# Performance work log

Hardware: AMD Instinct MI355X
Metric: run time of the kernel (lower is better)

The kernel has to match this reference:

```python
import jax, jax.numpy as jnp
import numpy as np
import math

B, S, D, H = 2, 2048, 1024, 16
DK = D // H


def setup_inputs() -> dict:
    key = jax.random.key(0)
    ks = jax.random.split(key, 12)
    std = 1.0 / math.sqrt(D)
    inp = {
        "q": jax.random.normal(ks[0], (B, S, D), jnp.float32),
        "k": jax.random.normal(ks[1], (B, S, D), jnp.float32),
        "v": jax.random.normal(ks[2], (B, S, D), jnp.float32),
        # causal mask, broadcast over batch and heads
        "mask": jnp.tril(jnp.ones((S, S), jnp.int32))[None, None, :, :],
        "wq": jax.random.normal(ks[3], (D, D), jnp.float32) * std,
        "bq": jax.random.normal(ks[4], (D,), jnp.float32) * std,
        "wk": jax.random.normal(ks[5], (D, D), jnp.float32) * std,
        "bk": jax.random.normal(ks[6], (D,), jnp.float32) * std,
        "wv": jax.random.normal(ks[7], (D, D), jnp.float32) * std,
        "bv": jax.random.normal(ks[8], (D,), jnp.float32) * std,
        "wo": jax.random.normal(ks[9], (D, D), jnp.float32) * std,
        "bo": jax.random.normal(ks[10], (D,), jnp.float32) * std,
    }
    return inp


def _split_heads(x):
    # [B,S,D] -> [B,H,S,DK]
    b, s, _ = x.shape
    return x.reshape(b, s, H, DK).transpose(0, 2, 1, 3)


def reference(q, k, v, mask, wq, bq, wk, bk, wv, bv, wo, bo):
    # nn.Linear: y = x @ W^T + b
    query = _split_heads(q @ wq.T + bq)
    key_h = _split_heads(k @ wk.T + bk)
    value = _split_heads(v @ wv.T + bv)

    scale = 1.0 / math.sqrt(DK)
    scores = jnp.einsum("bhqd,bhkd->bhqk", query, key_h) * scale  # [B,H,S,S]
    scores = jnp.where(mask == 0, jnp.float32(-1e9), scores)
    attn = jax.nn.softmax(scores, axis=-1)  # dropout p=0.0 -> identity

    x = jnp.einsum("bhqk,bhkd->bhqd", attn, value)  # [B,H,S,DK]
    x = x.transpose(0, 2, 1, 3).reshape(q.shape[0], -1, H * DK)  # [B,S,D]
    return x @ wo.T + bo
```

## Files before the change

### kernel.cpp

```cpp
#include <hip/hip_runtime.h>

#define B_SZ    2
#define S_LEN   2048
#define D_MODEL 1024
#define H_NUM   16
#define DK_H    64
#define M_ROWS  (B_SZ * S_LEN)

typedef __attribute__((ext_vector_type(8))) short  short8;
typedef __attribute__((ext_vector_type(4))) short  short4v;
typedef __attribute__((ext_vector_type(4))) float  floatx4;

__device__ __forceinline__ short f2b(float f) {
    union { float f; unsigned u; } x; x.f = f;
    unsigned u = x.u + 0x7fffu + ((x.u >> 16) & 1u);
    return (short)(u >> 16);
}

typedef __attribute__((address_space(1))) const unsigned int gu32;
typedef __attribute__((address_space(3))) unsigned int       lu32;
__device__ __forceinline__ void gload_lds16(const short* g, short* l) {
    __builtin_amdgcn_global_load_lds((gu32*)g, (lu32*)l, 16, 0, 0);
}

#define QSCALE 0.18033688011112042f
#define SM_SHIFT 12.0f

__global__ void cvt_all_kernel(const float* __restrict__ xq, const float* __restrict__ xk,
                               const float* __restrict__ xv, const float* __restrict__ wq,
                               const float* __restrict__ wk, const float* __restrict__ wv,
                               const float* __restrict__ wo,
                               short* __restrict__ oxq, short* __restrict__ oxk,
                               short* __restrict__ oxv, short* __restrict__ owq,
                               short* __restrict__ owk, short* __restrict__ owv,
                               short* __restrict__ owo)
{
    const int y = blockIdx.y;
    const float* in;
    short* out;
    switch (y) {
        case 0: in = xq; out = oxq; break;
        case 1: in = xk; out = oxk; break;
        case 2: in = xv; out = oxv; break;
        case 3: in = wq; out = owq; break;
        case 4: in = wk; out = owk; break;
        case 5: in = wv; out = owv; break;
        default: in = wo; out = owo; break;
    }
    int base = blockIdx.x * 1024 + threadIdx.x * 4;
    if (y < 3) {
        for (int p = 0; p < 4; ++p) {
            int i = base + p * 1048576;
            float4 v = *(const float4*)(in + i);
            short4v r;
            r[0] = f2b(v.x); r[1] = f2b(v.y); r[2] = f2b(v.z); r[3] = f2b(v.w);
            *(short4v*)(out + i) = r;
        }
    } else {
        int i = base;
        int n = i >> 10, k = i & 1023;
        float4 v = *(const float4*)(in + i);
        short4v r;
        r[0] = f2b(v.x); r[1] = f2b(v.y); r[2] = f2b(v.z); r[3] = f2b(v.w);
        *(short4v*)(out + (((n >> 4) * 128 + (k >> 3)) * 128 + (n & 15) * 8 + (k & 4))) = r;
    }
}

__global__ __launch_bounds__(256, 2)
void gemm_qkv_kernel(const short* __restrict__ xq, const short* __restrict__ xk,
                     const short* __restrict__ xv,
                     const short* __restrict__ wq, const short* __restrict__ wk,
                     const short* __restrict__ wv,
                     const float* __restrict__ bq, const float* __restrict__ bk,
                     const float* __restrict__ bv,
                     short* __restrict__ Qp, short* __restrict__ Kp, short* __restrict__ Vt)
{
    __shared__ short sa[128 * 32];

    const int which = blockIdx.y >> 3;
    const short* A    = (which == 0) ? xq : (which == 1) ? xk : xv;
    const short* W    = (which == 0) ? wq : (which == 1) ? wk : wv;
    const float* bias = (which == 0) ? bq : (which == 1) ? bk : bv;
    const float scale = (which == 0) ? QSCALE : 1.0f;

    const int nb = (blockIdx.y & 7) * 128;
    const int m0 = blockIdx.x * 128;
    const int t = threadIdx.x, wave = t >> 6, lane = t & 63;
    const int quad = lane >> 4, l16 = lane & 15;
    const int wm = (wave & 1) * 64, wn = (wave >> 1) * 64;

    const int r0 = t >> 2, cs = t & 3;
    const int c0 = cs ^ ((r0 >> 1) & 3);
    const short* Ab0 = A + (size_t)(m0 + r0) * D_MODEL + c0 * 8;
    const short* Ab1 = Ab0 + (size_t)64 * D_MODEL;
    short* sa0 = sa + t * 8;  short* sa1 = sa + 2048 + t * 8;

    int a_off[4];
#pragma unroll
    for (int i = 0; i < 4; ++i) {
        int ar = wm + i * 16 + l16;
        a_off[i] = ar * 32 + ((quad ^ ((ar >> 1) & 3)) * 8);
    }

    const short* Wt = W + ((size_t)((nb + wn) >> 4) * 128 + quad) * 128 + l16 * 8;

#define LOADB(dst, k0) do { _Pragma("unroll")                                  \
    for (int nt_ = 0; nt_ < 4; ++nt_)                                          \
        dst[nt_] = *(const short8*)(Wt + nt_ * 16384 + (k0) * 16); } while (0)

    short8 bfA[4], bfB[4];
    LOADB(bfA, 0);

    floatx4 acc[4][4] = {};
#pragma unroll 1
    for (int k0 = 0; k0 < D_MODEL; k0 += 64) {
        __syncthreads();
        gload_lds16(Ab0 + k0, sa0);
        gload_lds16(Ab1 + k0, sa1);
        __syncthreads();
        LOADB(bfB, k0 + 32);
#pragma unroll
        for (int mt = 0; mt < 4; ++mt) {
            short8 af = *(const short8*)(sa + a_off[mt]);
#pragma unroll
            for (int nt = 0; nt < 4; ++nt)
                acc[mt][nt] = __builtin_amdgcn_mfma_f32_16x16x32_bf16(af, bfA[nt], acc[mt][nt], 0, 0, 0);
        }
        __syncthreads();
        gload_lds16(Ab0 + k0 + 32, sa0);
        gload_lds16(Ab1 + k0 + 32, sa1);
        __syncthreads();
        if (k0 + 64 < D_MODEL) LOADB(bfA, k0 + 64);
#pragma unroll
        for (int mt = 0; mt < 4; ++mt) {
            short8 af = *(const short8*)(sa + a_off[mt]);
#pragma unroll
            for (int nt = 0; nt < 4; ++nt)
                acc[mt][nt] = __builtin_amdgcn_mfma_f32_16x16x32_bf16(af, bfB[nt], acc[mt][nt], 0, 0, 0);
        }
    }
#undef LOADB

#pragma unroll
    for (int nt = 0; nt < 4; ++nt) {
        int ncol = nb + wn + nt * 16 + l16;
        int h = ncol >> 6, dk = ncol & 63;
        float bv_ = bias[ncol];
#pragma unroll
        for (int mt = 0; mt < 4; ++mt) {
            int mrow0 = m0 + wm + mt * 16 + quad * 4;
            int bb = mrow0 >> 11, s0 = mrow0 & (S_LEN - 1);
            if (which < 2) {
                short* Out = (which == 0) ? Qp : Kp;
#pragma unroll
                for (int r = 0; r < 4; ++r) {
                    float v = (acc[mt][nt][r] + bv_) * scale;
                    Out[(((size_t)bb * H_NUM + h) * S_LEN + (s0 + r)) * DK_H + dk] = f2b(v);
                }
            } else {
                int Sb = s0 & ~63, sb0_ = s0 & 63;
                size_t rowbase = (((size_t)bb * H_NUM + h) * DK_H + dk) * S_LEN + Sb;
#pragma unroll
                for (int r = 0; r < 4; ++r) {
                    int cc = sb0_ + r;
                    Vt[rowbase + ((cc & 15) * 4 + (cc >> 4))] = f2b(acc[mt][nt][r] + bv_);
                }
            }
        }
    }
}

__global__ __launch_bounds__(512, 4)
void attn_kernel(const short* __restrict__ Qp, const short* __restrict__ Kp,
                 const short* __restrict__ Vt, short* __restrict__ Xa)
{
    __shared__ short kbuf[2][64 * 64];
    __shared__ short vbuf[2][64 * 64];
    __shared__ short pl[8][16 * 72];

    const int lin = (int)(blockIdx.x + 16 * blockIdx.y);
    const int bh = lin & 31;
    const int j8 = (lin >> 5) & 7;
    const int tile = (lin >> 8) ? (15 - j8) : j8;

    const int t = threadIdx.x, wave = t >> 6, lane = t & 63;
    const int quad = lane >> 4, l16 = lane & 15;

    const short* Qb  = Qp + (size_t)bh * S_LEN * DK_H;
    const short* Kb  = Kp + (size_t)bh * S_LEN * DK_H;
    const short* Vtb = Vt + (size_t)bh * DK_H * S_LEN;

    const int q0 = tile * 128 + wave * 16;
    const int my_ktimax = 2 * tile + (wave >> 2);
    const int ktb = 2 * tile + 1;

    const int r0 = t >> 3, cs = t & 7;
    const int c0 = cs ^ (r0 & 7);
    const short* Kg = Kb + r0 * DK_H + c0 * 8;
    const short* Vg = Vtb + (size_t)r0 * S_LEN + c0 * 8;
    short* kl0 = &kbuf[0][t * 8]; short* kl1 = &kbuf[1][t * 8];
    short* vl0 = &vbuf[0][t * 8]; short* vl1 = &vbuf[1][t * 8];

    short8 qf[2];
#pragma unroll
    for (int ks = 0; ks < 2; ++ks)
        qf[ks] = *(const short8*)(Qb + (size_t)(q0 + l16) * DK_H + ks * 32 + quad * 8);

    short8 bl = {};
    if (l16 == 0) {
#pragma unroll
        for (int j = 0; j < 8; ++j) bl[j] = (short)0x3F80;
    }

    int fo[4][2];
#pragma unroll
    for (int nt = 0; nt < 4; ++nt)
#pragma unroll
        for (int ks = 0; ks < 2; ++ks) {
            int row = nt * 16 + l16;
            fo[nt][ks] = row * 64 + (((ks * 4 + quad) ^ (l16 & 7)) * 8);
        }

    floatx4 o[4] = {};
    floatx4 ol = {};
    short* plw = &pl[wave][0];
    const int qg = q0 + quad * 4;

    gload_lds16(Kg, kl0);
    gload_lds16(Vg, vl0);
    __syncthreads();

    for (int kti = 0; kti <= ktb; ++kti) {
        const short* kb = (kti & 1) ? &kbuf[1][0] : &kbuf[0][0];
        const short* vb = (kti & 1) ? &vbuf[1][0] : &vbuf[0][0];
        const int kbase = kti * 64;

        if (kti < ktb) {
            gload_lds16(Kg + (size_t)(kbase + 64) * DK_H, (kti & 1) ? kl0 : kl1);
            gload_lds16(Vg + (kbase + 64),                (kti & 1) ? vl0 : vl1);
        }

        if (kti <= my_ktimax) {
            short8 bkf[4][2];
#pragma unroll
            for (int nt = 0; nt < 4; ++nt)
#pragma unroll
                for (int ks = 0; ks < 2; ++ks)
                    bkf[nt][ks] = *(const short8*)(kb + fo[nt][ks]);

            floatx4 sc[4] = {};
#pragma unroll
            for (int nt = 0; nt < 4; ++nt)
#pragma unroll
                for (int ks = 0; ks < 2; ++ks)
                    sc[nt] = __builtin_amdgcn_mfma_f32_16x16x32_bf16(qf[ks], bkf[nt][ks], sc[nt], 0, 0, 0);

            if (kti == my_ktimax) {
#pragma unroll
                for (int nt = 0; nt < 4; ++nt) {
                    int key = kbase + nt * 16 + l16;
#pragma unroll
                    for (int r = 0; r < 4; ++r)
                        if (key > qg + r) sc[nt][r] = -1e30f;
                }
            }

#pragma unroll
            for (int r = 0; r < 4; ++r) {
                union { float f; unsigned u; } a0, a1, a2, a3;
                a0.f = exp2f(sc[0][r] - SM_SHIFT);
                a1.f = exp2f(sc[1][r] - SM_SHIFT);
                a2.f = exp2f(sc[2][r] - SM_SHIFT);
                a3.f = exp2f(sc[3][r] - SM_SHIFT);
                uint2 d;
                d.x = (a1.u & 0xffff0000u) | (a0.u >> 16);
                d.y = (a3.u & 0xffff0000u) | (a2.u >> 16);
                *(uint2*)(plw + (quad * 4 + r) * 72 + l16 * 4) = d;
            }

            short8 ap0 = *(const short8*)(plw + l16 * 72 + quad * 8);
            short8 ap1 = *(const short8*)(plw + l16 * 72 + 32 + quad * 8);

            short8 bvf[4][2];
#pragma unroll
            for (int nt = 0; nt < 4; ++nt)
#pragma unroll
                for (int ks = 0; ks < 2; ++ks)
                    bvf[nt][ks] = *(const short8*)(vb + fo[nt][ks]);

#pragma unroll
            for (int nt = 0; nt < 4; ++nt) {
                o[nt] = __builtin_amdgcn_mfma_f32_16x16x32_bf16(ap0, bvf[nt][0], o[nt], 0, 0, 0);
                o[nt] = __builtin_amdgcn_mfma_f32_16x16x32_bf16(ap1, bvf[nt][1], o[nt], 0, 0, 0);
            }
            ol = __builtin_amdgcn_mfma_f32_16x16x32_bf16(ap0, bl, ol, 0, 0, 0);
            ol = __builtin_amdgcn_mfma_f32_16x16x32_bf16(ap1, bl, ol, 0, 0, 0);
        }

        __syncthreads();
    }

    const int b_ = bh >> 4, h = bh & 15;
#pragma unroll
    for (int r = 0; r < 4; ++r) {
        float lsum = __shfl(ol[r], (lane & 48));
        float rinv = 1.0f / lsum;
        int srow = qg + r;
#pragma unroll
        for (int nt = 0; nt < 4; ++nt) {
            int col = h * 64 + nt * 16 + l16;
            Xa[((size_t)b_ * S_LEN + srow) * D_MODEL + col] = f2b(o[nt][r] * rinv);
        }
    }
}

__global__ __launch_bounds__(256, 2)
void gemm_out_kernel(const short* __restrict__ A, const short* __restrict__ W,
                     const float* __restrict__ bias, float* __restrict__ out)
{
    __shared__ short sa[128 * 32];

    const int nb = blockIdx.y * 64;
    const int m0 = blockIdx.x * 128;
    const int t = threadIdx.x, wave = t >> 6, lane = t & 63;
    const int quad = lane >> 4, l16 = lane & 15;
    const int wm = (wave & 1) * 64, wn = (wave >> 1) * 32;

    const int r0 = t >> 2, cs = t & 3;
    const int c0 = cs ^ ((r0 >> 1) & 3);
    const short* Ab0 = A + (size_t)(m0 + r0) * D_MODEL + c0 * 8;
    const short* Ab1 = Ab0 + (size_t)64 * D_MODEL;
    short* sa0 = sa + t * 8;  short* sa1 = sa + 2048 + t * 8;

    int a_off[4];
#pragma unroll
    for (int i = 0; i < 4; ++i) {
        int ar = wm + i * 16 + l16;
        a_off[i] = ar * 32 + ((quad ^ ((ar >> 1) & 3)) * 8);
    }

    const short* Wt = W + ((size_t)((nb + wn) >> 4) * 128 + quad) * 128 + l16 * 8;

#define LOADB2(dst, k0) do { _Pragma("unroll")                                 \
    for (int nt_ = 0; nt_ < 2; ++nt_)                                          \
        dst[nt_] = *(const short8*)(Wt + nt_ * 16384 + (k0) * 16); } while (0)

    short8 bfA[2], bfB[2];
    LOADB2(bfA, 0);

    floatx4 acc[4][2] = {};
#pragma unroll 1
    for (int k0 = 0; k0 < D_MODEL; k0 += 64) {
        __syncthreads();
        gload_lds16(Ab0 + k0, sa0);
        gload_lds16(Ab1 + k0, sa1);
        __syncthreads();
        LOADB2(bfB, k0 + 32);
#pragma unroll
        for (int mt = 0; mt < 4; ++mt) {
            short8 af = *(const short8*)(sa + a_off[mt]);
#pragma unroll
            for (int nt = 0; nt < 2; ++nt)
                acc[mt][nt] = __builtin_amdgcn_mfma_f32_16x16x32_bf16(af, bfA[nt], acc[mt][nt], 0, 0, 0);
        }
        __syncthreads();
        gload_lds16(Ab0 + k0 + 32, sa0);
        gload_lds16(Ab1 + k0 + 32, sa1);
        __syncthreads();
        if (k0 + 64 < D_MODEL) LOADB2(bfA, k0 + 64);
#pragma unroll
        for (int mt = 0; mt < 4; ++mt) {
            short8 af = *(const short8*)(sa + a_off[mt]);
#pragma unroll
            for (int nt = 0; nt < 2; ++nt)
                acc[mt][nt] = __builtin_amdgcn_mfma_f32_16x16x32_bf16(af, bfB[nt], acc[mt][nt], 0, 0, 0);
        }
    }
#undef LOADB2

#pragma unroll
    for (int nt = 0; nt < 2; ++nt) {
        int ncol = nb + wn + nt * 16 + l16;
        float bv_ = bias[ncol];
#pragma unroll
        for (int mt = 0; mt < 4; ++mt) {
            int mrow0 = m0 + wm + mt * 16 + quad * 4;
#pragma unroll
            for (int r = 0; r < 4; ++r)
                out[(size_t)(mrow0 + r) * D_MODEL + ncol] = acc[mt][nt][r] + bv_;
        }
    }
}

extern "C" void kernel_launch(void* const* d_in, const int* in_sizes, int n_in,
                              void* d_out, int out_size, void* d_ws, size_t ws_size,
                              hipStream_t stream)
{
    (void)in_sizes; (void)n_in; (void)out_size; (void)ws_size;
    const float* q  = (const float*)d_in[0];
    const float* k  = (const float*)d_in[1];
    const float* v  = (const float*)d_in[2];
    const float* wq = (const float*)d_in[4];
    const float* bq = (const float*)d_in[5];
    const float* wk = (const float*)d_in[6];
    const float* bk = (const float*)d_in[7];
    const float* wv = (const float*)d_in[8];
    const float* bv = (const float*)d_in[9];
    const float* wo = (const float*)d_in[10];
    const float* bo = (const float*)d_in[11];
    float* out = (float*)d_out;

    const size_t XE = (size_t)M_ROWS * D_MODEL;
    const size_t WE = (size_t)D_MODEL * D_MODEL;
    short* ws_  = (short*)d_ws;
    short* xq_b = ws_;
    short* xk_b = xq_b + XE;
    short* xv_b = xk_b + XE;
    short* wq_b = xv_b + XE;
    short* wk_b = wq_b + WE;
    short* wv_b = wk_b + WE;
    short* wo_b = wv_b + WE;
    short* Qp   = wo_b + WE;
    short* Kp   = Qp + XE;
    short* Vt   = Kp + XE;
    short* Xa   = xq_b;

    dim3 blk(256);
    cvt_all_kernel<<<dim3(1024, 7), blk, 0, stream>>>(
        q, k, v, wq, wk, wv, wo, xq_b, xk_b, xv_b, wq_b, wk_b, wv_b, wo_b);

    gemm_qkv_kernel<<<dim3(M_ROWS / 128, 24), blk, 0, stream>>>(
        xq_b, xk_b, xv_b, wq_b, wk_b, wv_b, bq, bk, bv, Qp, Kp, Vt);

    attn_kernel<<<dim3(16, B_SZ * H_NUM), dim3(512), 0, stream>>>(Qp, Kp, Vt, Xa);

    gemm_out_kernel<<<dim3(M_ROWS / 128, D_MODEL / 64), blk, 0, stream>>>(Xa, wo_b, bo, out);
}
```

Baseline: 232.1 us.

## Double-buffer A tiles in LDS for projection GEMMs and coalesce weight repack

The QKV and output GEMMs now stage the full 64-wide K slab of A into one of two LDS buffers with an XOR swizzle. The next slab is prefetched while the current one is consumed, which replaces four barriers per iteration with one. The weight conversion kernel is also rewritten so each thread reads 8 contiguous floats and writes a contiguous short8 in the packed layout. In exchange, LDS use per block grows fourfold, which could limit occupancy.

```diff
diff --git a/kernel.cpp b/kernel.cpp
--- a/kernel.cpp
+++ b/kernel.cpp
@@ -47,8 +47,8 @@
         case 5: in = wv; out = owv; break;
         default: in = wo; out = owo; break;
     }
-    int base = blockIdx.x * 1024 + threadIdx.x * 4;
     if (y < 3) {
+        int base = blockIdx.x * 1024 + threadIdx.x * 4;
         for (int p = 0; p < 4; ++p) {
             int i = base + p * 1048576;
             float4 v = *(const float4*)(in + i);
@@ -57,12 +57,18 @@
             *(short4v*)(out + i) = r;
         }
     } else {
-        int i = base;
-        int n = i >> 10, k = i & 1023;
-        float4 v = *(const float4*)(in + i);
-        short4v r;
-        r[0] = f2b(v.x); r[1] = f2b(v.y); r[2] = f2b(v.z); r[3] = f2b(v.w);
-        *(short4v*)(out + (((n >> 4) * 128 + (k >> 3)) * 128 + (n & 15) * 8 + (k & 4))) = r;
+        int f = blockIdx.x * 256 + (int)threadIdx.x;
+        if (blockIdx.x < 512) {
+            int n4 = f >> 11, rem = f & 2047;
+            int k8 = rem >> 4, nl = rem & 15;
+            const float* src = in + (size_t)(n4 * 16 + nl) * D_MODEL + k8 * 8;
+            float4 v0 = *(const float4*)(src);
+            float4 v1 = *(const float4*)(src + 4);
+            short8 r;
+            r[0] = f2b(v0.x); r[1] = f2b(v0.y); r[2] = f2b(v0.z); r[3] = f2b(v0.w);
+            r[4] = f2b(v1.x); r[5] = f2b(v1.y); r[6] = f2b(v1.z); r[7] = f2b(v1.w);
+            *(short8*)(out + (size_t)f * 8) = r;
+        }
     }
 }
 
@@ -75,7 +81,7 @@
                      const float* __restrict__ bv,
                      short* __restrict__ Qp, short* __restrict__ Kp, short* __restrict__ Vt)
 {
-    __shared__ short sa[128 * 32];
+    __shared__ short sa[2][128 * 64];
 
     const int which = blockIdx.y >> 3;
     const short* A    = (which == 0) ? xq : (which == 1) ? xk : xv;
@@ -89,17 +95,24 @@
     const int quad = lane >> 4, l16 = lane & 15;
     const int wm = (wave & 1) * 64, wn = (wave >> 1) * 64;
 
-    const int r0 = t >> 2, cs = t & 3;
-    const int c0 = cs ^ ((r0 >> 1) & 3);
-    const short* Ab0 = A + (size_t)(m0 + r0) * D_MODEL + c0 * 8;
-    const short* Ab1 = Ab0 + (size_t)64 * D_MODEL;
-    short* sa0 = sa + t * 8;  short* sa1 = sa + 2048 + t * 8;
-
-    int a_off[4];
+    const int rs = t >> 3;
+    const int cl = (t & 7) ^ (rs & 7);
+    const short* Asrc = A + (size_t)(m0 + rs) * D_MODEL + cl * 8;
+    short* sd0 = &sa[0][t * 8];
+    short* sd1 = &sa[1][t * 8];
+
+#define STAGE_A(dst, k0) do { _Pragma("unroll")                                \
+    for (int j_ = 0; j_ < 4; ++j_)                                             \
+        gload_lds16(Asrc + (size_t)j_ * 32 * D_MODEL + (k0),                   \
+                    (dst) + j_ * 2048); } while (0)
+
+    int a_off[4][2];
 #pragma unroll
     for (int i = 0; i < 4; ++i) {
         int ar = wm + i * 16 + l16;
-        a_off[i] = ar * 32 + ((quad ^ ((ar >> 1) & 3)) * 8);
+#pragma unroll
+        for (int ks = 0; ks < 2; ++ks)
+            a_off[i][ks] = ar * 64 + (((ks * 4 + quad) ^ (ar & 7)) * 8);
     }
 
     const short* Wt = W + ((size_t)((nb + wn) >> 4) * 128 + quad) * 128 + l16 * 8;
@@ -109,36 +122,38 @@
         dst[nt_] = *(const short8*)(Wt + nt_ * 16384 + (k0) * 16); } while (0)
 
     short8 bfA[4], bfB[4];
+    STAGE_A(sd0, 0);
     LOADB(bfA, 0);
+    __syncthreads();
 
     floatx4 acc[4][4] = {};
 #pragma unroll 1
     for (int k0 = 0; k0 < D_MODEL; k0 += 64) {
+        const int p = (k0 >> 6) & 1;
+        const short* cur = &sa[p][0];
+        if (k0 + 64 < D_MODEL) STAGE_A(p ? sd0 : sd1, k0 + 64);
+        LOADB(bfB, k0 + 32);
+
+        short8 af[4][2];
+#pragma unroll
+        for (int mt = 0; mt < 4; ++mt) {
+            af[mt][0] = *(const short8*)(cur + a_off[mt][0]);
+            af[mt][1] = *(const short8*)(cur + a_off[mt][1]);
+        }
+#pragma unroll
+        for (int mt = 0; mt < 4; ++mt)
+#pragma unroll
+            for (int nt = 0; nt < 4; ++nt)
+                acc[mt][nt] = __builtin_amdgcn_mfma_f32_16x16x32_bf16(af[mt][0], bfA[nt], acc[mt][nt], 0, 0, 0);
+        if (k0 + 64 < D_MODEL) LOADB(bfA, k0 + 64);
+#pragma unroll
+        for (int mt = 0; mt < 4; ++mt)
+#pragma unroll
+            for (int nt = 0; nt < 4; ++nt)
+                acc[mt][nt] = __builtin_amdgcn_mfma_f32_16x16x32_bf16(af[mt][1], bfB[nt], acc[mt][nt], 0, 0, 0);
         __syncthreads();
-        gload_lds16(Ab0 + k0, sa0);
-        gload_lds16(Ab1 + k0, sa1);
-        __syncthreads();
-        LOADB(bfB, k0 + 32);
-#pragma unroll
-        for (int mt = 0; mt < 4; ++mt) {
-            short8 af = *(const short8*)(sa + a_off[mt]);
-#pragma unroll
-            for (int nt = 0; nt < 4; ++nt)
-                acc[mt][nt] = __builtin_amdgcn_mfma_f32_16x16x32_bf16(af, bfA[nt], acc[mt][nt], 0, 0, 0);
-        }
-        __syncthreads();
-        gload_lds16(Ab0 + k0 + 32, sa0);
-        gload_lds16(Ab1 + k0 + 32, sa1);
-        __syncthreads();
-        if (k0 + 64 < D_MODEL) LOADB(bfA, k0 + 64);
-#pragma unroll
-        for (int mt = 0; mt < 4; ++mt) {
-            short8 af = *(const short8*)(sa + a_off[mt]);
-#pragma unroll
-            for (int nt = 0; nt < 4; ++nt)
-                acc[mt][nt] = __builtin_amdgcn_mfma_f32_16x16x32_bf16(af, bfB[nt], acc[mt][nt], 0, 0, 0);
-        }
-    }
+    }
+#undef STAGE_A
 #undef LOADB
 
 #pragma unroll
@@ -318,7 +333,7 @@
 void gemm_out_kernel(const short* __restrict__ A, const short* __restrict__ W,
                      const float* __restrict__ bias, float* __restrict__ out)
 {
-    __shared__ short sa[128 * 32];
+    __shared__ short sa[2][128 * 64];
 
     const int nb = blockIdx.y * 64;
     const int m0 = blockIdx.x * 128;
@@ -326,17 +341,24 @@
     const int quad = lane >> 4, l16 = lane & 15;
     const int wm = (wave & 1) * 64, wn = (wave >> 1) * 32;
 
-    const int r0 = t >> 2, cs = t & 3;
-    const int c0 = cs ^ ((r0 >> 1) & 3);
-    const short* Ab0 = A + (size_t)(m0 + r0) * D_MODEL + c0 * 8;
-    const short* Ab1 = Ab0 + (size_t)64 * D_MODEL;
-    short* sa0 = sa + t * 8;  short* sa1 = sa + 2048 + t * 8;
-
-    int a_off[4];
+    const int rs = t >> 3;
+    const int cl = (t & 7) ^ (rs & 7);
+    const short* Asrc = A + (size_t)(m0 + rs) * D_MODEL + cl * 8;
+    short* sd0 = &sa[0][t * 8];
+    short* sd1 = &sa[1][t * 8];
+
+#define STAGE_A(dst, k0) do { _Pragma("unroll")                                \
+    for (int j_ = 0; j_ < 4; ++j_)                                             \
+        gload_lds16(Asrc + (size_t)j_ * 32 * D_MODEL + (k0),                   \
+                    (dst) + j_ * 2048); } while (0)
+
+    int a_off[4][2];
 #pragma unroll
     for (int i = 0; i < 4; ++i) {
         int ar = wm + i * 16 + l16;
-        a_off[i] = ar * 32 + ((quad ^ ((ar >> 1) & 3)) * 8);
+#pragma unroll
+        for (int ks = 0; ks < 2; ++ks)
+            a_off[i][ks] = ar * 64 + (((ks * 4 + quad) ^ (ar & 7)) * 8);
     }
 
     const short* Wt = W + ((size_t)((nb + wn) >> 4) * 128 + quad) * 128 + l16 * 8;
@@ -346,36 +368,38 @@
         dst[nt_] = *(const short8*)(Wt + nt_ * 16384 + (k0) * 16); } while (0)
 
     short8 bfA[2], bfB[2];
+    STAGE_A(sd0, 0);
     LOADB2(bfA, 0);
+    __syncthreads();
 
     floatx4 acc[4][2] = {};
 #pragma unroll 1
     for (int k0 = 0; k0 < D_MODEL; k0 += 64) {
+        const int p = (k0 >> 6) & 1;
+        const short* cur = &sa[p][0];
+        if (k0 + 64 < D_MODEL) STAGE_A(p ? sd0 : sd1, k0 + 64);
+        LOADB2(bfB, k0 + 32);
+
+        short8 af[4][2];
+#pragma unroll
+        for (int mt = 0; mt < 4; ++mt) {
+            af[mt][0] = *(const short8*)(cur + a_off[mt][0]);
+            af[mt][1] = *(const short8*)(cur + a_off[mt][1]);
+        }
+#pragma unroll
+        for (int mt = 0; mt < 4; ++mt)
+#pragma unroll
+            for (int nt = 0; nt < 2; ++nt)
+                acc[mt][nt] = __builtin_amdgcn_mfma_f32_16x16x32_bf16(af[mt][0], bfA[nt], acc[mt][nt], 0, 0, 0);
+        if (k0 + 64 < D_MODEL) LOADB2(bfA, k0 + 64);
+#pragma unroll
+        for (int mt = 0; mt < 4; ++mt)
+#pragma unroll
+            for (int nt = 0; nt < 2; ++nt)
+                acc[mt][nt] = __builtin_amdgcn_mfma_f32_16x16x32_bf16(af[mt][1], bfB[nt], acc[mt][nt], 0, 0, 0);
         __syncthreads();
-        gload_lds16(Ab0 + k0, sa0);
-        gload_lds16(Ab1 + k0, sa1);
-        __syncthreads();
-        LOADB2(bfB, k0 + 32);
-#pragma unroll
-        for (int mt = 0; mt < 4; ++mt) {
-            short8 af = *(const short8*)(sa + a_off[mt]);
-#pragma unroll
-            for (int nt = 0; nt < 2; ++nt)
-                acc[mt][nt] = __builtin_amdgcn_mfma_f32_16x16x32_bf16(af, bfA[nt], acc[mt][nt], 0, 0, 0);
-        }
-        __syncthreads();
-        gload_lds16(Ab0 + k0 + 32, sa0);
-        gload_lds16(Ab1 + k0 + 32, sa1);
-        __syncthreads();
-        if (k0 + 64 < D_MODEL) LOADB2(bfA, k0 + 64);
-#pragma unroll
-        for (int mt = 0; mt < 4; ++mt) {
-            short8 af = *(const short8*)(sa + a_off[mt]);
-#pragma unroll
-            for (int nt = 0; nt < 2; ++nt)
-                acc[mt][nt] = __builtin_amdgcn_mfma_f32_16x16x32_bf16(af, bfB[nt], acc[mt][nt], 0, 0, 0);
-        }
-    }
+    }
+#undef STAGE_A
 #undef LOADB2
 
 #pragma unroll
```

Measured after the change: 218.9 us. 1.06x faster.
